# Optimization experiments

Hardware: AMD Instinct MI355X
Metric: run time of the kernel (lower is better)

## Reference

```python
import jax, jax.numpy as jnp
import numpy as np

VOCAB, INPUT, HIDDEN = 50000, 512, 1024
BATCH, MAX_LEN = 64, 256


def setup_inputs() -> dict:
    key = jax.random.key(0)
    ks = jax.random.split(key, 16)
    s = 0.02
    return {
        "last_output": jax.random.randint(ks[0], (BATCH,), 0, VOCAB),
        "last_hidden": jax.random.normal(ks[1], (BATCH, HIDDEN), jnp.float32),
        "encoder_outputs": jax.random.normal(ks[2], (MAX_LEN, BATCH, HIDDEN), jnp.float32),
        # embedding table (padding_idx=0 just means row 0 is a pad row; math is a plain gather)
        "embedding": jax.random.uniform(ks[3], (VOCAB, INPUT), jnp.float32, -0.25, 0.25),
        # concat attention: Linear(2H -> H) and v [H]
        "attn_W": jax.random.normal(ks[4], (HIDDEN, 2 * HIDDEN), jnp.float32) * s,
        "attn_b": jnp.zeros((HIDDEN,), jnp.float32),
        "v": jax.random.normal(ks[5], (HIDDEN,), jnp.float32) * s,
        # GRU (single layer): input size = INPUT + HIDDEN, gate order r,z,n (torch order)
        "W_ih": jax.random.normal(ks[6], (3 * HIDDEN, INPUT + HIDDEN), jnp.float32) * s,
        "W_hh": jax.random.uniform(ks[7], (3 * HIDDEN, HIDDEN), jnp.float32, -0.01, 0.01),
        "b_ih": jnp.zeros((3 * HIDDEN,), jnp.float32),
        "b_hh": jnp.zeros((3 * HIDDEN,), jnp.float32),
        # output projection Linear(2H -> vocab)
        "out_W": jax.random.normal(ks[8], (VOCAB, 2 * HIDDEN), jnp.float32) * s,
        "out_b": jnp.zeros((VOCAB,), jnp.float32),
    }


def reference(last_output, last_hidden, encoder_outputs, embedding,
              attn_W, attn_b, v, W_ih, W_hh, b_ih, b_hh, out_W, out_b):
    T, B, H = encoder_outputs.shape
    # --- embedding lookup: [B, INPUT]
    emb = embedding[last_output]

    # --- concat (Bahdanau-style, no tanh in original) attention, vectorized over T
    hid = jnp.broadcast_to(last_hidden[None], (T, B, H))
    cat = jnp.concatenate([hid, encoder_outputs], axis=-1)          # [T,B,2H]
    energy = jnp.einsum('tbk,hk->tbh', cat, attn_W) + attn_b        # [T,B,H]
    scores = jnp.einsum('tbh,h->bt', energy, v)                     # [B,T]
    attn = jax.nn.softmax(scores, axis=1)                           # [B,T]

    # --- context: [B,H]
    context = jnp.einsum('bt,tbh->bh', attn, encoder_outputs)

    # --- single GRU step (torch gate order r,z,n)
    x = jnp.concatenate([emb, context], axis=-1)                    # [B, INPUT+H]
    gi = x @ W_ih.T + b_ih                                          # [B,3H]
    gh = last_hidden @ W_hh.T + b_hh                                # [B,3H]
    i_r, i_z, i_n = jnp.split(gi, 3, axis=-1)
    h_r, h_z, h_n = jnp.split(gh, 3, axis=-1)
    r = jax.nn.sigmoid(i_r + h_r)
    z = jax.nn.sigmoid(i_z + h_z)
    n = jnp.tanh(i_n + r * h_n)
    h_new = (1.0 - z) * n + z * last_hidden                         # [B,H]

    # --- output projection + log_softmax over vocab
    logits = jnp.concatenate([h_new, context], axis=-1) @ out_W.T + out_b
    logp = jax.nn.log_softmax(logits, axis=-1)                      # [B,VOCAB]
    return logp, h_new
```

## Files before the change

kernel.cpp:

```cpp
#include <hip/hip_runtime.h>
#include <cstddef>

#define VOCAB  50000
#define INPUT  512
#define HIDDEN 1024
#define BATCH  64
#define MAXLEN 256
#define NBLK   625

typedef float  f32x4 __attribute__((ext_vector_type(4)));
typedef __bf16 bf16x8 __attribute__((ext_vector_type(8)));

__device__ __forceinline__ bf16x8 cvt8(float4 a, float4 b) {
    bf16x8 r;
    r[0] = (__bf16)a.x; r[1] = (__bf16)a.y; r[2] = (__bf16)a.z; r[3] = (__bf16)a.w;
    r[4] = (__bf16)b.x; r[5] = (__bf16)b.y; r[6] = (__bf16)b.z; r[7] = (__bf16)b.w;
    return r;
}

__global__ void k_u2_part(const float* __restrict__ attn_W, const float* __restrict__ v,
                          float* __restrict__ u2p) {
    int bid = blockIdx.x, tid = threadIdx.x;
    int hq = bid >> 4, kc = bid & 15;
    int kl = tid & 63, hg = tid >> 6;
    int k = kc * 64 + kl;
    float acc = 0.f;
    int h0 = hq * 256 + hg * 64;
#pragma unroll 8
    for (int h = h0; h < h0 + 64; ++h)
        acc += v[h] * attn_W[(size_t)h * (2 * HIDDEN) + HIDDEN + k];
    __shared__ float red[4][64];
    red[hg][kl] = acc;
    __syncthreads();
    if (tid < 64)
        u2p[hq * 1024 + kc * 64 + tid] =
            red[0][tid] + red[1][tid] + red[2][tid] + red[3][tid];
}

__global__ __launch_bounds__(256) void k_att(const float* __restrict__ enc,
                                             const float* __restrict__ u2p,
                                             float* __restrict__ mpart,
                                             float* __restrict__ lpart,
                                             float* __restrict__ ctxp) {
    int bid = blockIdx.x, tid = threadIdx.x;
    int b = bid >> 2, tq = bid & 3, t0 = tq * 64;
    __shared__ float u2s[1024];
    __shared__ float erow[4][1024];
    __shared__ float sc[4];
    for (int i = tid; i < 1024; i += 256)
        u2s[i] = u2p[i] + u2p[1024 + i] + u2p[2048 + i] + u2p[3072 + i];
    __syncthreads();
    int w = tid >> 6, lane = tid & 63;
    float m = -INFINITY, l = 0.f;
    float4 acc = {0.f, 0.f, 0.f, 0.f};
    int h4 = tid * 4;
    for (int r = 0; r < 16; ++r) {
        int t = t0 + r * 4 + w;
        const float* row = enc + ((size_t)t * BATCH + b) * HIDDEN;
        float partial = 0.f;
#pragma unroll
        for (int i = 0; i < 4; ++i) {
            int h = lane * 4 + i * 256;
            float4 e = *(const float4*)(row + h);
            *(float4*)(&erow[w][h]) = e;
            float4 u = *(const float4*)(&u2s[h]);
            partial += e.x * u.x + e.y * u.y + e.z * u.z + e.w * u.w;
        }
#pragma unroll
        for (int off = 32; off; off >>= 1) partial += __shfl_down(partial, off, 64);
        if (lane == 0) sc[w] = partial;
        __syncthreads();
        float s0 = sc[0], s1 = sc[1], s2 = sc[2], s3 = sc[3];
#pragma unroll
        for (int q = 0; q < 4; ++q) {
            float s = (q == 0) ? s0 : (q == 1) ? s1 : (q == 2) ? s2 : s3;
            float mn = fmaxf(m, s);
            float corr = expf(m - mn);
            float p = expf(s - mn);
            float4 e = *(const float4*)(&erow[q][h4]);
            acc.x = acc.x * corr + p * e.x;
            acc.y = acc.y * corr + p * e.y;
            acc.z = acc.z * corr + p * e.z;
            acc.w = acc.w * corr + p * e.w;
            l = l * corr + p;
            m = mn;
        }
        __syncthreads();
    }
    int o = b * 4 + tq;
    *(float4*)(ctxp + (size_t)o * 1024 + h4) = acc;
    if (tid == 0) { mpart[o] = m; lpart[o] = l; }
}

__global__ void k_att_comb(const float* __restrict__ mpart, const float* __restrict__ lpart,
                           const float* __restrict__ ctxp,
                           const int* __restrict__ last_output,
                           const float* __restrict__ embedding,
                           const float* __restrict__ hid,
                           __bf16* __restrict__ x_bf, __bf16* __restrict__ hid_bf,
                           __bf16* __restrict__ y_bf) {
    int b = blockIdx.x >> 2, hc = blockIdx.x & 3, tid = threadIdx.x;
    float m0 = mpart[b * 4 + 0], m1 = mpart[b * 4 + 1];
    float m2 = mpart[b * 4 + 2], m3 = mpart[b * 4 + 3];
    float M = fmaxf(fmaxf(m0, m1), fmaxf(m2, m3));
    float w0 = expf(m0 - M), w1 = expf(m1 - M), w2 = expf(m2 - M), w3 = expf(m3 - M);
    float denom = lpart[b * 4 + 0] * w0 + lpart[b * 4 + 1] * w1 +
                  lpart[b * 4 + 2] * w2 + lpart[b * 4 + 3] * w3;
    float inv = 1.f / denom;
    int h = hc * 256 + tid;
    const float* cp = ctxp + (size_t)b * 4096 + h;
    float c = (w0 * cp[0] + w1 * cp[1024] + w2 * cp[2048] + w3 * cp[3072]) * inv;
    x_bf[b * 1536 + INPUT + h]  = (__bf16)c;
    y_bf[b * 2048 + HIDDEN + h] = (__bf16)c;
    if (hc < 2)
        x_bf[b * 1536 + hc * 256 + tid] =
            (__bf16)embedding[(size_t)last_output[b] * INPUT + hc * 256 + tid];
    hid_bf[b * HIDDEN + hc * 256 + tid] = (__bf16)hid[b * HIDDEN + hc * 256 + tid];
}

__device__ __forceinline__ void gemm_tile(const float* __restrict__ W,
                                          const float* __restrict__ bias,
                                          const __bf16* __restrict__ A,
                                          float* __restrict__ out,
                                          int N, int K, int jt, int tid) {
    int wid = tid >> 6, lane = tid & 63;
    int j  = jt * 16 + (lane & 15);
    int kg = (lane >> 4) * 8;
    int kchunk = K >> 2;
    int kbeg = wid * kchunk, kend = kbeg + kchunk;
    const float*  wrow = W + (size_t)j * K;
    const __bf16* arow = A + (size_t)(lane & 15) * K;
    f32x4 acc[4] = {};
    for (int k0 = kbeg; k0 < kend; k0 += 32) {
        int kk = k0 + kg;
        float4 w0 = *(const float4*)(wrow + kk);
        float4 w1 = *(const float4*)(wrow + kk + 4);
        bf16x8 bw = cvt8(w0, w1);
#pragma unroll
        for (int mt = 0; mt < 4; ++mt) {
            bf16x8 av = *(const bf16x8*)(arow + (size_t)mt * 16 * K + kk);
            acc[mt] = __builtin_amdgcn_mfma_f32_16x16x32_bf16(av, bw, acc[mt], 0, 0, 0);
        }
    }
    __shared__ float lds[4][1024];
#pragma unroll
    for (int mt = 0; mt < 4; ++mt)
#pragma unroll
        for (int r = 0; r < 4; ++r) {
            int m = mt * 16 + (lane >> 4) * 4 + r;
            lds[wid][m * 16 + (lane & 15)] = acc[mt][r];
        }
    __syncthreads();
#pragma unroll
    for (int o = tid; o < 1024; o += 256) {
        float s = lds[0][o] + lds[1][o] + lds[2][o] + lds[3][o];
        int m = o >> 4, jl = o & 15;
        out[(size_t)m * N + jt * 16 + jl] = s + bias[jt * 16 + jl];
    }
}

__global__ __launch_bounds__(256) void k_gemm_gru(const float* __restrict__ W_ih,
                                                  const float* __restrict__ b_ih,
                                                  const __bf16* __restrict__ x_bf,
                                                  float* __restrict__ Gi,
                                                  const float* __restrict__ W_hh,
                                                  const float* __restrict__ b_hh,
                                                  const __bf16* __restrict__ hid_bf,
                                                  float* __restrict__ Gh) {
    int bid = blockIdx.x, tid = threadIdx.x;
    if (bid < 192) gemm_tile(W_ih, b_ih, x_bf,  Gi, 3072, 1536, bid,       tid);
    else           gemm_tile(W_hh, b_hh, hid_bf, Gh, 3072, 1024, bid - 192, tid);
}

__global__ void k_combine(const float* __restrict__ Gi, const float* __restrict__ Gh,
                          const float* __restrict__ hid, float* __restrict__ hnew_out,
                          __bf16* __restrict__ y_bf) {
    int idx = blockIdx.x * 256 + threadIdx.x;
    int b = idx >> 10, h = idx & 1023;
    const float* gi = Gi + (size_t)b * 3072;
    const float* gh = Gh + (size_t)b * 3072;
    float r  = 1.f / (1.f + expf(-(gi[h] + gh[h])));
    float z  = 1.f / (1.f + expf(-(gi[1024 + h] + gh[1024 + h])));
    float n  = tanhf(gi[2048 + h] + r * gh[2048 + h]);
    float hp = hid[b * HIDDEN + h];
    float hn = (1.f - z) * n + z * hp;
    hnew_out[b * HIDDEN + h] = hn;
    y_bf[b * 2048 + h] = (__bf16)hn;
}

__global__ __launch_bounds__(256) void k_gemv(const float* __restrict__ W,
                                              const float* __restrict__ bias,
                                              const __bf16* __restrict__ A,
                                              float* __restrict__ out,
                                              float* __restrict__ mw,
                                              float* __restrict__ sw) {
    int bid = blockIdx.x, tid = threadIdx.x;
    int wid = tid >> 6, lane = tid & 63;
    int kg = (lane >> 4) * 8;
    int kbeg = wid * 512;
    int j0 = bid * 80 + (lane & 15);
    const float* wrow0 = W + (size_t)(j0     ) * 2048;
    const float* wrow1 = W + (size_t)(j0 + 16) * 2048;
    const float* wrow2 = W + (size_t)(j0 + 32) * 2048;
    const float* wrow3 = W + (size_t)(j0 + 48) * 2048;
    const float* wrow4 = W + (size_t)(j0 + 64) * 2048;
    const __bf16* arow = A + (size_t)(lane & 15) * 2048;
    f32x4 acc[5][4] = {};
    for (int k0 = kbeg; k0 < kbeg + 512; k0 += 32) {
        int kk = k0 + kg;
        bf16x8 bw0 = cvt8(*(const float4*)(wrow0 + kk), *(const float4*)(wrow0 + kk + 4));
        bf16x8 bw1 = cvt8(*(const float4*)(wrow1 + kk), *(const float4*)(wrow1 + kk + 4));
        bf16x8 bw2 = cvt8(*(const float4*)(wrow2 + kk), *(const float4*)(wrow2 + kk + 4));
        bf16x8 bw3 = cvt8(*(const float4*)(wrow3 + kk), *(const float4*)(wrow3 + kk + 4));
        bf16x8 bw4 = cvt8(*(const float4*)(wrow4 + kk), *(const float4*)(wrow4 + kk + 4));
#pragma unroll
        for (int mt = 0; mt < 4; ++mt) {
            bf16x8 av = *(const bf16x8*)(arow + (size_t)mt * 16 * 2048 + kk);
            acc[0][mt] = __builtin_amdgcn_mfma_f32_16x16x32_bf16(av, bw0, acc[0][mt], 0, 0, 0);
            acc[1][mt] = __builtin_amdgcn_mfma_f32_16x16x32_bf16(av, bw1, acc[1][mt], 0, 0, 0);
            acc[2][mt] = __builtin_amdgcn_mfma_f32_16x16x32_bf16(av, bw2, acc[2][mt], 0, 0, 0);
            acc[3][mt] = __builtin_amdgcn_mfma_f32_16x16x32_bf16(av, bw3, acc[3][mt], 0, 0, 0);
            acc[4][mt] = __builtin_amdgcn_mfma_f32_16x16x32_bf16(av, bw4, acc[4][mt], 0, 0, 0);
        }
    }
    __shared__ float lds[4][1024];
    float Mreg = -INFINITY, Sreg = 0.f;
#pragma unroll
    for (int u = 0; u < 5; ++u) {
        if (u) __syncthreads();
#pragma unroll
        for (int mt = 0; mt < 4; ++mt)
#pragma unroll
            for (int r = 0; r < 4; ++r) {
                int m = mt * 16 + (lane >> 4) * 4 + r;
                lds[wid][m * 16 + (lane & 15)] = acc[u][mt][r];
            }
        __syncthreads();
#pragma unroll
        for (int o = tid; o < 1024; o += 256) {
            float s = lds[0][o] + lds[1][o] + lds[2][o] + lds[3][o];
            int m = o >> 4, jl = o & 15;
            int jj = bid * 80 + u * 16 + jl;
            s += bias[jj];
            out[(size_t)m * VOCAB + jj] = s;
            lds[0][o] = s;
        }
        __syncthreads();
        if (tid < 64) {
            float mx = -INFINITY;
#pragma unroll
            for (int jl = 0; jl < 16; ++jl) mx = fmaxf(mx, lds[0][tid * 16 + jl]);
            float se = 0.f;
#pragma unroll
            for (int jl = 0; jl < 16; ++jl) se += expf(lds[0][tid * 16 + jl] - mx);
            float M2 = fmaxf(Mreg, mx);
            Sreg = Sreg * expf(Mreg - M2) + se * expf(mx - M2);
            Mreg = M2;
        }
    }
    if (tid < 64) {
        mw[(size_t)tid * NBLK + bid] = Mreg;
        sw[(size_t)tid * NBLK + bid] = Sreg;
    }
}

__global__ __launch_bounds__(256) void k_lse_fused(float* __restrict__ logits,
                                                   const float* __restrict__ mw,
                                                   const float* __restrict__ sw) {
    int bid = blockIdx.x, tid = threadIdx.x;
    int b = bid / 13, c = bid % 13;
    const float* mrow = mw + (size_t)b * NBLK;
    const float* srow = sw + (size_t)b * NBLK;
    __shared__ float red[256];
    float m = -INFINITY;
    for (int i = tid; i < NBLK; i += 256) m = fmaxf(m, mrow[i]);
    red[tid] = m; __syncthreads();
    for (int off = 128; off; off >>= 1) { if (tid < off) red[tid] = fmaxf(red[tid], red[tid + off]); __syncthreads(); }
    m = red[0]; __syncthreads();
    float s = 0.f;
    for (int i = tid; i < NBLK; i += 256) s += srow[i] * expf(mrow[i] - m);
    red[tid] = s; __syncthreads();
    for (int off = 128; off; off >>= 1) { if (tid < off) red[tid] += red[tid + off]; __syncthreads(); }
    float lse = m + logf(red[0]);
    int base = c * 4096;
    int len  = min(4096, VOCAB - base);
    float* row = logits + (size_t)b * VOCAB + base;
    for (int i = tid * 4; i < len; i += 1024) {
        float4 x = *(float4*)(row + i);
        x.x -= lse; x.y -= lse; x.z -= lse; x.w -= lse;
        *(float4*)(row + i) = x;
    }
}

extern "C" void kernel_launch(void* const* d_in, const int* in_sizes, int n_in,
                              void* d_out, int out_size, void* d_ws, size_t ws_size,
                              hipStream_t stream) {
    const int*   last_output = (const int*)  d_in[0];
    const float* last_hidden = (const float*)d_in[1];
    const float* enc         = (const float*)d_in[2];
    const float* embedding   = (const float*)d_in[3];
    const float* attn_W      = (const float*)d_in[4];
    const float* v           = (const float*)d_in[6];
    const float* W_ih        = (const float*)d_in[7];
    const float* W_hh        = (const float*)d_in[8];
    const float* b_ih        = (const float*)d_in[9];
    const float* b_hh        = (const float*)d_in[10];
    const float* out_W       = (const float*)d_in[11];
    const float* out_b       = (const float*)d_in[12];

    float* out_logp = (float*)d_out;
    float* out_hnew = (float*)d_out + (size_t)BATCH * VOCAB;

    char* ws = (char*)d_ws;
    float*  u2p     = (float*) (ws + 0);
    float*  mpart   = (float*) (ws + 16384);
    float*  lpart   = (float*) (ws + 17408);
    float*  ctxp    = (float*) (ws + 18432);
    __bf16* x_bf    = (__bf16*)(ws + 1067008);
    __bf16* hid_bf  = (__bf16*)(ws + 1263616);
    __bf16* y_bf    = (__bf16*)(ws + 1394688);
    float*  Gi      = (float*) (ws + 1656832);
    float*  Gh      = (float*) (ws + 2443264);
    float*  mw      = (float*) (ws + 3229696);
    float*  sw      = (float*) (ws + 3389696);

    k_u2_part  <<<64,   256, 0, stream>>>(attn_W, v, u2p);
    k_att      <<<256,  256, 0, stream>>>(enc, u2p, mpart, lpart, ctxp);
    k_att_comb <<<256,  256, 0, stream>>>(mpart, lpart, ctxp, last_output, embedding,
                                          last_hidden, x_bf, hid_bf, y_bf);
    k_gemm_gru <<<384,  256, 0, stream>>>(W_ih, b_ih, x_bf, Gi, W_hh, b_hh, hid_bf, Gh);
    k_combine  <<<256,  256, 0, stream>>>(Gi, Gh, last_hidden, out_hnew, y_bf);
    k_gemv     <<<NBLK, 256, 0, stream>>>(out_W, out_b, y_bf, out_logp, mw, sw);
    k_lse_fused<<<832,  256, 0, stream>>>(out_logp, mw, sw);
}
```

Before: 183.1 us.

## Double-buffer encoder rows in attention and move bf16 packing into u2 kernel

The attention kernel now prefetches the next group of encoder rows into registers and double-buffers the shared row and score arrays. Each iteration needs one barrier instead of two, and global loads overlap the softmax-weighted accumulation. The embedding gather and the hidden-state bf16 conversion move out of the combine kernel into extra blocks of the u2 kernel, which runs alongside the small u2 reduction. This doubles the attention kernel's shared memory and adds register pressure, which could reduce occupancy.

New measurement: 180.1 us. About the same (-1.6%).

```diff
diff --git a/kernel.cpp b/kernel.cpp
--- a/kernel.cpp
+++ b/kernel.cpp
@@ -18,23 +18,39 @@
     return r;
 }
 
-__global__ void k_u2_part(const float* __restrict__ attn_W, const float* __restrict__ v,
-                          float* __restrict__ u2p) {
-    int bid = blockIdx.x, tid = threadIdx.x;
-    int hq = bid >> 4, kc = bid & 15;
-    int kl = tid & 63, hg = tid >> 6;
-    int k = kc * 64 + kl;
-    float acc = 0.f;
-    int h0 = hq * 256 + hg * 64;
+__global__ void k_u2_pack(const float* __restrict__ attn_W, const float* __restrict__ v,
+                          float* __restrict__ u2p,
+                          const int* __restrict__ last_output,
+                          const float* __restrict__ embedding,
+                          const float* __restrict__ hid,
+                          __bf16* __restrict__ x_bf, __bf16* __restrict__ hid_bf) {
+    int bid = blockIdx.x, tid = threadIdx.x;
+    if (bid < 64) {
+        int hq = bid >> 4, kc = bid & 15;
+        int kl = tid & 63, hg = tid >> 6;
+        int k = kc * 64 + kl;
+        float acc = 0.f;
+        int h0 = hq * 256 + hg * 64;
 #pragma unroll 8
-    for (int h = h0; h < h0 + 64; ++h)
-        acc += v[h] * attn_W[(size_t)h * (2 * HIDDEN) + HIDDEN + k];
-    __shared__ float red[4][64];
-    red[hg][kl] = acc;
-    __syncthreads();
-    if (tid < 64)
-        u2p[hq * 1024 + kc * 64 + tid] =
-            red[0][tid] + red[1][tid] + red[2][tid] + red[3][tid];
+        for (int h = h0; h < h0 + 64; ++h)
+            acc += v[h] * attn_W[(size_t)h * (2 * HIDDEN) + HIDDEN + k];
+        __shared__ float red[4][64];
+        red[hg][kl] = acc;
+        __syncthreads();
+        if (tid < 64)
+            u2p[hq * 1024 + kc * 64 + tid] =
+                red[0][tid] + red[1][tid] + red[2][tid] + red[3][tid];
+    } else {
+        int idx = (bid - 64) * 256 + tid;
+        if (idx < 64 * INPUT) {
+            int b = idx >> 9, k = idx & 511;
+            x_bf[b * 1536 + k] = (__bf16)embedding[(size_t)last_output[b] * INPUT + k];
+        } else {
+            idx -= 64 * INPUT;
+            int b = idx >> 10, h = idx & 1023;
+            hid_bf[b * HIDDEN + h] = (__bf16)hid[b * HIDDEN + h];
+        }
+    }
 }
 
 __global__ __launch_bounds__(256) void k_att(const float* __restrict__ enc,
@@ -45,39 +61,58 @@
     int bid = blockIdx.x, tid = threadIdx.x;
     int b = bid >> 2, tq = bid & 3, t0 = tq * 64;
     __shared__ float u2s[1024];
-    __shared__ float erow[4][1024];
-    __shared__ float sc[4];
+    __shared__ float erow[2][4][1024];
+    __shared__ float sc[2][4];
     for (int i = tid; i < 1024; i += 256)
         u2s[i] = u2p[i] + u2p[1024 + i] + u2p[2048 + i] + u2p[3072 + i];
-    __syncthreads();
     int w = tid >> 6, lane = tid & 63;
+    int h4 = tid * 4;
     float m = -INFINITY, l = 0.f;
     float4 acc = {0.f, 0.f, 0.f, 0.f};
-    int h4 = tid * 4;
+    float4 e0, e1, e2, e3;
+    {
+        const float* row = enc + ((size_t)(t0 + w) * BATCH + b) * HIDDEN + lane * 4;
+        e0 = *(const float4*)(row);
+        e1 = *(const float4*)(row + 256);
+        e2 = *(const float4*)(row + 512);
+        e3 = *(const float4*)(row + 768);
+    }
+    __syncthreads();
+    {
+        float4 u0 = *(const float4*)(&u2s[lane * 4]);
+        float4 u1 = *(const float4*)(&u2s[lane * 4 + 256]);
+        float4 u2v = *(const float4*)(&u2s[lane * 4 + 512]);
+        float4 u3 = *(const float4*)(&u2s[lane * 4 + 768]);
+        float partial = e0.x*u0.x + e0.y*u0.y + e0.z*u0.z + e0.w*u0.w
+                      + e1.x*u1.x + e1.y*u1.y + e1.z*u1.z + e1.w*u1.w
+                      + e2.x*u2v.x + e2.y*u2v.y + e2.z*u2v.z + e2.w*u2v.w
+                      + e3.x*u3.x + e3.y*u3.y + e3.z*u3.z + e3.w*u3.w;
+        *(float4*)(&erow[0][w][lane * 4      ]) = e0;
+        *(float4*)(&erow[0][w][lane * 4 + 256]) = e1;
+        *(float4*)(&erow[0][w][lane * 4 + 512]) = e2;
+        *(float4*)(&erow[0][w][lane * 4 + 768]) = e3;
+#pragma unroll
+        for (int off = 32; off; off >>= 1) partial += __shfl_down(partial, off, 64);
+        if (lane == 0) sc[0][w] = partial;
+    }
+    __syncthreads();
     for (int r = 0; r < 16; ++r) {
-        int t = t0 + r * 4 + w;
-        const float* row = enc + ((size_t)t * BATCH + b) * HIDDEN;
-        float partial = 0.f;
-#pragma unroll
-        for (int i = 0; i < 4; ++i) {
-            int h = lane * 4 + i * 256;
-            float4 e = *(const float4*)(row + h);
-            *(float4*)(&erow[w][h]) = e;
-            float4 u = *(const float4*)(&u2s[h]);
-            partial += e.x * u.x + e.y * u.y + e.z * u.z + e.w * u.w;
-        }
-#pragma unroll
-        for (int off = 32; off; off >>= 1) partial += __shfl_down(partial, off, 64);
-        if (lane == 0) sc[w] = partial;
-        __syncthreads();
-        float s0 = sc[0], s1 = sc[1], s2 = sc[2], s3 = sc[3];
+        int cur = r & 1, nxt = cur ^ 1;
+        if (r < 15) {
+            const float* row = enc + ((size_t)(t0 + (r + 1) * 4 + w) * BATCH + b) * HIDDEN + lane * 4;
+            e0 = *(const float4*)(row);
+            e1 = *(const float4*)(row + 256);
+            e2 = *(const float4*)(row + 512);
+            e3 = *(const float4*)(row + 768);
+        }
+        float s0 = sc[cur][0], s1 = sc[cur][1], s2 = sc[cur][2], s3 = sc[cur][3];
 #pragma unroll
         for (int q = 0; q < 4; ++q) {
             float s = (q == 0) ? s0 : (q == 1) ? s1 : (q == 2) ? s2 : s3;
             float mn = fmaxf(m, s);
             float corr = expf(m - mn);
             float p = expf(s - mn);
-            float4 e = *(const float4*)(&erow[q][h4]);
+            float4 e = *(const float4*)(&erow[cur][q][h4]);
             acc.x = acc.x * corr + p * e.x;
             acc.y = acc.y * corr + p * e.y;
             acc.z = acc.z * corr + p * e.z;
@@ -85,6 +120,23 @@
             l = l * corr + p;
             m = mn;
         }
+        if (r < 15) {
+            float4 u0 = *(const float4*)(&u2s[lane * 4]);
+            float4 u1 = *(const float4*)(&u2s[lane * 4 + 256]);
+            float4 u2v = *(const float4*)(&u2s[lane * 4 + 512]);
+            float4 u3 = *(const float4*)(&u2s[lane * 4 + 768]);
+            float partial = e0.x*u0.x + e0.y*u0.y + e0.z*u0.z + e0.w*u0.w
+                          + e1.x*u1.x + e1.y*u1.y + e1.z*u1.z + e1.w*u1.w
+                          + e2.x*u2v.x + e2.y*u2v.y + e2.z*u2v.z + e2.w*u2v.w
+                          + e3.x*u3.x + e3.y*u3.y + e3.z*u3.z + e3.w*u3.w;
+            *(float4*)(&erow[nxt][w][lane * 4      ]) = e0;
+            *(float4*)(&erow[nxt][w][lane * 4 + 256]) = e1;
+            *(float4*)(&erow[nxt][w][lane * 4 + 512]) = e2;
+            *(float4*)(&erow[nxt][w][lane * 4 + 768]) = e3;
+#pragma unroll
+            for (int off = 32; off; off >>= 1) partial += __shfl_down(partial, off, 64);
+            if (lane == 0) sc[nxt][w] = partial;
+        }
         __syncthreads();
     }
     int o = b * 4 + tq;
@@ -94,11 +146,7 @@
 
 __global__ void k_att_comb(const float* __restrict__ mpart, const float* __restrict__ lpart,
                            const float* __restrict__ ctxp,
-                           const int* __restrict__ last_output,
-                           const float* __restrict__ embedding,
-                           const float* __restrict__ hid,
-                           __bf16* __restrict__ x_bf, __bf16* __restrict__ hid_bf,
-                           __bf16* __restrict__ y_bf) {
+                           __bf16* __restrict__ x_bf, __bf16* __restrict__ y_bf) {
     int b = blockIdx.x >> 2, hc = blockIdx.x & 3, tid = threadIdx.x;
     float m0 = mpart[b * 4 + 0], m1 = mpart[b * 4 + 1];
     float m2 = mpart[b * 4 + 2], m3 = mpart[b * 4 + 3];
@@ -112,10 +160,6 @@
     float c = (w0 * cp[0] + w1 * cp[1024] + w2 * cp[2048] + w3 * cp[3072]) * inv;
     x_bf[b * 1536 + INPUT + h]  = (__bf16)c;
     y_bf[b * 2048 + HIDDEN + h] = (__bf16)c;
-    if (hc < 2)
-        x_bf[b * 1536 + hc * 256 + tid] =
-            (__bf16)embedding[(size_t)last_output[b] * INPUT + hc * 256 + tid];
-    hid_bf[b * HIDDEN + hc * 256 + tid] = (__bf16)hid[b * HIDDEN + hc * 256 + tid];
 }
 
 __device__ __forceinline__ void gemm_tile(const float* __restrict__ W,
@@ -324,10 +368,10 @@
     float*  mw      = (float*) (ws + 3229696);
     float*  sw      = (float*) (ws + 3389696);
 
-    k_u2_part  <<<64,   256, 0, stream>>>(attn_W, v, u2p);
+    k_u2_pack  <<<448,  256, 0, stream>>>(attn_W, v, u2p, last_output, embedding,
+                                          last_hidden, x_bf, hid_bf);
     k_att      <<<256,  256, 0, stream>>>(enc, u2p, mpart, lpart, ctxp);
-    k_att_comb <<<256,  256, 0, stream>>>(mpart, lpart, ctxp, last_output, embedding,
-                                          last_hidden, x_bf, hid_bf, y_bf);
+    k_att_comb <<<256,  256, 0, stream>>>(mpart, lpart, ctxp, x_bf, y_bf);
     k_gemm_gru <<<384,  256, 0, stream>>>(W_ih, b_ih, x_bf, Gi, W_hh, b_hh, hid_bf, Gh);
     k_combine  <<<256,  256, 0, stream>>>(Gi, Gh, last_hidden, out_hnew, y_bf);
     k_gemv     <<<NBLK, 256, 0, stream>>>(out_W, out_b, y_bf, out_logp, mw, sw);
```
